# Optimization experiments

Measured on AMD Instinct MI355X. Metric: run time of the kernel, lower is better.

The kernel has to match this reference:

```python
import jax, jax.numpy as jnp
import numpy as np

EMBED_DIM = 256
SEQ_LEN = 4096
BATCH = 8
ALPHA = 0.99


def setup_inputs() -> dict:
    key = jax.random.key(0)
    k_x, k_w, k_b = jax.random.split(key, 3)
    x = jax.random.normal(k_x, (BATCH, SEQ_LEN, EMBED_DIM), dtype=jnp.float32)
    # nn.Linear(embed_dim, 3*embed_dim): store as [d, 3d] so y = x @ Wqkv + bqkv
    Wqkv = jax.random.normal(k_w, (EMBED_DIM, 3 * EMBED_DIM), dtype=jnp.float32) * (EMBED_DIM ** -0.5)
    bqkv = jax.random.normal(k_b, (3 * EMBED_DIM,), dtype=jnp.float32) * 0.02
    return {"x": x, "Wqkv": Wqkv, "bqkv": bqkv}


def reference(x, Wqkv, bqkv):
    bs, sl, d = x.shape
    qkv = x @ Wqkv + bqkv                      # [bs, sl, 3d]
    q, k, v = jnp.split(qkv, 3, axis=-1)       # each [bs, sl, d]
    # causal * exponential-decay mask: M[i, j] = alpha**(i-j) for j <= i else 0
    i = jnp.arange(sl, dtype=jnp.float32)
    M = jnp.where(i[:, None] >= i[None, :],
                  jnp.power(jnp.float32(ALPHA), i[:, None] - i[None, :]),
                  0.0)                          # [sl, sl]
    scores = jnp.einsum('bqd,bkd->bqk', q, k) / jnp.sqrt(jnp.float32(d))
    out = jnp.einsum('bqk,bkd->bqd', scores * M, v)
    return out
```

## Files before the change

kernel.cpp:

```cpp
#include <hip/hip_runtime.h>

typedef __bf16 bf16x8 __attribute__((ext_vector_type(8)));
typedef float f32x4 __attribute__((ext_vector_type(4)));
typedef unsigned short u16;
typedef unsigned int u32;
typedef u16 u16x4 __attribute__((ext_vector_type(4)));
typedef u16 u16x8 __attribute__((ext_vector_type(8)));

#define L2ALPHA (-0.014499569f)
#define WIN 1024

static __device__ __forceinline__ u16 f2bf(float f) {
    u32 u = __builtin_bit_cast(u32, f);
    return (u16)((u + 0x7FFFu + ((u >> 16) & 1u)) >> 16);
}

static __device__ __forceinline__ void gl2lds16(const void* g, void* l) {
    __builtin_amdgcn_global_load_lds(
        (const __attribute__((address_space(1))) u32*)g,
        (__attribute__((address_space(3))) u32*)l, 16, 0, 0);
}

__global__ __launch_bounds__(256, 2) void proj_kernel(
        const float* __restrict__ x, const float* __restrict__ Wq,
        const float* __restrict__ bias,
        u16* __restrict__ qb, u16* __restrict__ kb, u16* __restrict__ vb)
{
    __shared__ __align__(16) u16 Bs[32 * 128 * 8];
    __shared__ __align__(16) u16 As[4][32 * 40];

    const int tid = threadIdx.x, lane = tid & 63, w = tid >> 6;
    const int l = blockIdx.x;
    const int nb = l % 6;
    const int mt = l / 6;
    const int m0 = mt * 128, n0 = nb * 128;
    const int m = lane & 15, quad = lane >> 4;

    {
        const int col = tid & 127;
        const int khalf = tid >> 7;
        #pragma unroll
        for (int s = 0; s < 32; ++s) {
            int k0 = (khalf + 2 * s) * 4;
            u16x4 h;
            #pragma unroll
            for (int i = 0; i < 4; ++i)
                h[i] = f2bf(Wq[(k0 + i) * 768 + n0 + col]);
            *(u16x4*)&Bs[((k0 >> 3) * 128 + col) * 8 + (k0 & 7)] = h;
        }
    }
    __syncthreads();

    const int r = lane & 31, h = lane >> 5;
    const float* xrow = x + (size_t)(m0 + w * 32 + r) * 256 + h * 16;
    u16* As_w = &As[w][0];

    f32x4 acc[2][8];
    #pragma unroll
    for (int rt = 0; rt < 2; ++rt)
        #pragma unroll
        for (int ct = 0; ct < 8; ++ct)
            acc[rt][ct] = f32x4{0.f, 0.f, 0.f, 0.f};

    float4 g0 = *(const float4*)(xrow + 0);
    float4 g1 = *(const float4*)(xrow + 4);
    float4 g2 = *(const float4*)(xrow + 8);
    float4 g3 = *(const float4*)(xrow + 12);

    for (int kt = 0; kt < 8; ++kt) {
        u16x8 ha, hb;
        ha[0]=f2bf(g0.x); ha[1]=f2bf(g0.y); ha[2]=f2bf(g0.z); ha[3]=f2bf(g0.w);
        ha[4]=f2bf(g1.x); ha[5]=f2bf(g1.y); ha[6]=f2bf(g1.z); ha[7]=f2bf(g1.w);
        hb[0]=f2bf(g2.x); hb[1]=f2bf(g2.y); hb[2]=f2bf(g2.z); hb[3]=f2bf(g2.w);
        hb[4]=f2bf(g3.x); hb[5]=f2bf(g3.y); hb[6]=f2bf(g3.z); hb[7]=f2bf(g3.w);
        *(u16x8*)&As_w[r * 40 + h * 16]     = ha;
        *(u16x8*)&As_w[r * 40 + h * 16 + 8] = hb;

        if (kt < 7) {
            const float* xn = xrow + (kt + 1) * 32;
            g0 = *(const float4*)(xn + 0);
            g1 = *(const float4*)(xn + 4);
            g2 = *(const float4*)(xn + 8);
            g3 = *(const float4*)(xn + 12);
        }

        asm volatile("s_waitcnt lgkmcnt(0)" ::: "memory");

        bf16x8 af[2], bfr[8];
        #pragma unroll
        for (int rt = 0; rt < 2; ++rt)
            af[rt] = *(const bf16x8*)&As_w[(rt * 16 + m) * 40 + quad * 8];
        #pragma unroll
        for (int ct = 0; ct < 8; ++ct)
            bfr[ct] = *(const bf16x8*)&Bs[((kt * 4 + quad) * 128 + ct * 16 + m) * 8];
        #pragma unroll
        for (int rt = 0; rt < 2; ++rt)
            #pragma unroll
            for (int ct = 0; ct < 8; ++ct)
                acc[rt][ct] = __builtin_amdgcn_mfma_f32_16x16x32_bf16(
                    af[rt], bfr[ct], acc[rt][ct], 0, 0, 0);
    }

    const int b = m0 >> 12;
    const int jbase = (m0 & 4095) + w * 32;
    const int d0 = (nb & 1) * 128;

    if (nb < 2) {
        #pragma unroll
        for (int rt = 0; rt < 2; ++rt)
            #pragma unroll
            for (int ct = 0; ct < 8; ++ct) {
                int coll = ct * 16 + m;
                float bv = bias[d0 + coll];
                #pragma unroll
                for (int rr = 0; rr < 4; ++rr) {
                    int row = m0 + w * 32 + rt * 16 + quad * 4 + rr;
                    qb[(size_t)row * 256 + d0 + coll] = f2bf((acc[rt][ct][rr] + bv) * 0.0625f);
                }
            }
    } else if (nb < 4) {
        #pragma unroll
        for (int rt = 0; rt < 2; ++rt)
            #pragma unroll
            for (int ct = 0; ct < 8; ++ct) {
                int d = d0 + ct * 16 + m;
                float bv = bias[256 + d];
                int k8 = d >> 5, qk = (d >> 3) & 3, e = d & 7;
                #pragma unroll
                for (int rr = 0; rr < 4; ++rr) {
                    int j = jbase + rt * 16 + quad * 4 + rr;
                    int jt = j >> 5, jj = j & 31;
                    kb[((((size_t)(b * 128 + jt) * 2 + (jj & 1)) * 8 + k8) * 64 + qk * 16 + (jj >> 1)) * 8 + e]
                        = f2bf(acc[rt][ct][rr] + bv);
                }
            }
    } else {
        #pragma unroll
        for (int rt = 0; rt < 2; ++rt)
            #pragma unroll
            for (int ct = 0; ct < 8; ++ct) {
                int d = d0 + ct * 16 + m;
                float bv = bias[512 + d];
                int dt = d >> 4, mv = d & 15;
                int j = jbase + rt * 16 + quad * 4;
                int jt = j >> 5, qv = (j >> 3) & 3, e0 = j & 7;
                u16x4 hv;
                #pragma unroll
                for (int rr = 0; rr < 4; ++rr) hv[rr] = f2bf(acc[rt][ct][rr] + bv);
                *(u16x4*)&vb[(((size_t)(b * 128 + jt) * 16 + dt) * 64 + qv * 16 + mv) * 8 + e0] = hv;
            }
    }
}

__global__ __launch_bounds__(512, 2) void attn_kernel(
        const u16* __restrict__ qb, const u16* __restrict__ kb,
        const u16* __restrict__ vb, float* __restrict__ out)
{
    __shared__ __align__(16) u16 KV[2][2][16384];
    __shared__ __align__(16) u16 Ps[8 * 32 * 40];

    const int tid = threadIdx.x, lane = tid & 63, w = tid >> 6;
    const int wp = w & 3, par = w >> 2;
    const int l = blockIdx.x;
    const int b = l & 7;
    const int m0 = (l >> 3) * 128;
    const int qrow0 = m0 + wp * 32;
    const int m = lane & 15, quad = lane >> 4;
    const size_t rowbase = (size_t)b * 4096;
    const size_t pbase = (size_t)b * 128;

    bf16x8 qf[2][8];
    #pragma unroll
    for (int rg = 0; rg < 2; ++rg)
        #pragma unroll
        for (int k8 = 0; k8 < 8; ++k8)
            qf[rg][k8] = *(const bf16x8*)(qb + (rowbase + qrow0 + rg * 16 + m) * 256 + k8 * 32 + quad * 8);

    float Arow[2][4];
    #pragma unroll
    for (int rg = 0; rg < 2; ++rg)
        #pragma unroll
        for (int rr = 0; rr < 4; ++rr)
            Arow[rg][rr] = __builtin_amdgcn_exp2f((float)(rg * 16 + quad * 4 + rr) * L2ALPHA);
    const float Em0 = __builtin_amdgcn_exp2f((float)(-2 * m) * L2ALPHA);
    const float Em1 = __builtin_amdgcn_exp2f((float)(-2 * m - 1) * L2ALPHA);

    f32x4 acc[2][16];
    #pragma unroll
    for (int rg = 0; rg < 2; ++rg)
        #pragma unroll
        for (int dt = 0; dt < 16; ++dt)
            acc[rg][dt] = f32x4{0.f, 0.f, 0.f, 0.f};

    int t0 = (m0 - WIN) >> 5; if (t0 < 0) t0 = 0;
    const int t1 = (m0 >> 5) + 3;
    const int nIter = (t1 - t0 + 2) >> 1;

    {
        const u16* kpA = kb + (pbase + t0) * 8192;
        const u16* vpA = vb + (pbase + t0) * 8192;
        const u16* kpB = kpA + 8192;
        const u16* vpB = vpA + 8192;
        #pragma unroll
        for (int s = 0; s < 2; ++s) {
            int c = tid + 512 * s;
            gl2lds16(kpA + (size_t)c * 8, &KV[0][0][c * 8]);
            gl2lds16(vpA + (size_t)c * 8, &KV[0][0][8192 + c * 8]);
            gl2lds16(kpB + (size_t)c * 8, &KV[0][1][c * 8]);
            gl2lds16(vpB + (size_t)c * 8, &KV[0][1][8192 + c * 8]);
        }
    }

    int p = 0;
    for (int it = 0; it < nIter; ++it) {
        __syncthreads();
        if (it + 1 < nIter) {
            const int ta = t0 + 2 * (it + 1);
            const bool haveB = (ta + 1 <= t1);
            const u16* kpA = kb + (pbase + ta) * 8192;
            const u16* vpA = vb + (pbase + ta) * 8192;
            #pragma unroll
            for (int s = 0; s < 2; ++s) {
                int c = tid + 512 * s;
                gl2lds16(kpA + (size_t)c * 8, &KV[p ^ 1][0][c * 8]);
                gl2lds16(vpA + (size_t)c * 8, &KV[p ^ 1][0][8192 + c * 8]);
                if (haveB) {
                    gl2lds16(kpA + 8192 + (size_t)c * 8, &KV[p ^ 1][1][c * 8]);
                    gl2lds16(vpA + 8192 + (size_t)c * 8, &KV[p ^ 1][1][8192 + c * 8]);
                }
            }
        }

        const int t = t0 + 2 * it + par;
        const int j0 = t * 32;
        if (t <= t1 && j0 <= qrow0 + 31 && j0 + (WIN + 31) >= qrow0) {
            const u16* Kt = &KV[p][par][0];
            const u16* Vt = &KV[p][par][8192];

            const float base = __builtin_amdgcn_exp2f((float)(qrow0 - j0) * L2ALPHA);
            const float C0 = base * Em0, C1 = base * Em1;
            const bool diag = (j0 == qrow0);

            f32x4 sA0{0.f,0.f,0.f,0.f}, sA1{0.f,0.f,0.f,0.f};
            f32x4 sB0{0.f,0.f,0.f,0.f}, sB1{0.f,0.f,0.f,0.f};
            #pragma unroll
            for (int k8 = 0; k8 < 8; ++k8) {
                bf16x8 bf0 = *(const bf16x8*)&Kt[(k8 * 64 + lane) * 8];
                sA0 = __builtin_amdgcn_mfma_f32_16x16x32_bf16(qf[0][k8], bf0, sA0, 0, 0, 0);
                sA1 = __builtin_amdgcn_mfma_f32_16x16x32_bf16(qf[1][k8], bf0, sA1, 0, 0, 0);
            }
            #pragma unroll
            for (int k8 = 0; k8 < 8; ++k8) {
                bf16x8 bf1 = *(const bf16x8*)&Kt[((8 + k8) * 64 + lane) * 8];
                sB0 = __builtin_amdgcn_mfma_f32_16x16x32_bf16(qf[0][k8], bf1, sB0, 0, 0, 0);
                sB1 = __builtin_amdgcn_mfma_f32_16x16x32_bf16(qf[1][k8], bf1, sB1, 0, 0, 0);
            }

            if (diag) {
                #pragma unroll
                for (int rg = 0; rg < 2; ++rg) {
                    f32x4 sh0 = rg ? sA1 : sA0;
                    f32x4 sh1 = rg ? sB1 : sB0;
                    #pragma unroll
                    for (int rr = 0; rr < 4; ++rr) {
                        int ioff = rg * 16 + quad * 4 + rr;
                        int dd0 = ioff - 2 * m;
                        float w0 = (dd0 >= 0) ? Arow[rg][rr] * C0 : 0.0f;
                        float w1 = (dd0 >= 1) ? Arow[rg][rr] * C1 : 0.0f;
                        int rowb = (w * 32 + ioff) * 40;
                        u32 pv = (u32)f2bf(sh0[rr] * w0) | ((u32)f2bf(sh1[rr] * w1) << 16);
                        *(u32*)&Ps[rowb + 2 * m] = pv;
                    }
                }
            } else {
                #pragma unroll
                for (int rg = 0; rg < 2; ++rg) {
                    f32x4 sh0 = rg ? sA1 : sA0;
                    f32x4 sh1 = rg ? sB1 : sB0;
                    #pragma unroll
                    for (int rr = 0; rr < 4; ++rr) {
                        int ioff = rg * 16 + quad * 4 + rr;
                        float w0 = Arow[rg][rr] * C0;
                        float w1 = Arow[rg][rr] * C1;
                        int rowb = (w * 32 + ioff) * 40;
                        u32 pv = (u32)f2bf(sh0[rr] * w0) | ((u32)f2bf(sh1[rr] * w1) << 16);
                        *(u32*)&Ps[rowb + 2 * m] = pv;
                    }
                }
            }
            asm volatile("s_waitcnt lgkmcnt(0)" ::: "memory");

            bf16x8 pa0 = *(const bf16x8*)&Ps[(w * 32 + m) * 40 + quad * 8];
            bf16x8 pa1 = *(const bf16x8*)&Ps[(w * 32 + 16 + m) * 40 + quad * 8];

            #pragma unroll
            for (int dt = 0; dt < 16; ++dt) {
                bf16x8 vf = *(const bf16x8*)&Vt[(dt * 64 + lane) * 8];
                acc[0][dt] = __builtin_amdgcn_mfma_f32_16x16x32_bf16(pa0, vf, acc[0][dt], 0, 0, 0);
                acc[1][dt] = __builtin_amdgcn_mfma_f32_16x16x32_bf16(pa1, vf, acc[1][dt], 0, 0, 0);
            }
        }
        p ^= 1;
    }

    __syncthreads();
    float* Comb = (float*)&KV[0][0][0];
    if (par == 1) {
        float* dst = Comb + (size_t)wp * 8192 + lane * 128;
        #pragma unroll
        for (int rg = 0; rg < 2; ++rg)
            #pragma unroll
            for (int dt = 0; dt < 16; ++dt) {
                int idx = rg * 16 + dt;
                *(f32x4*)(dst + (idx ^ (lane & 7)) * 4) = acc[rg][dt];
            }
    }
    __syncthreads();
    if (par == 0) {
        const float* src = Comb + (size_t)wp * 8192 + lane * 128;
        #pragma unroll
        for (int rg = 0; rg < 2; ++rg)
            #pragma unroll
            for (int dt = 0; dt < 16; ++dt) {
                int idx = rg * 16 + dt;
                f32x4 o = acc[rg][dt] + *(const f32x4*)(src + (idx ^ (lane & 7)) * 4);
                #pragma unroll
                for (int rr = 0; rr < 4; ++rr)
                    out[(rowbase + qrow0 + rg * 16 + quad * 4 + rr) * 256 + dt * 16 + m] = o[rr];
            }
    }
}

extern "C" void kernel_launch(void* const* d_in, const int* in_sizes, int n_in,
                              void* d_out, int out_size, void* d_ws, size_t ws_size,
                              hipStream_t stream) {
    (void)in_sizes; (void)n_in; (void)out_size; (void)ws_size;
    const float* x    = (const float*)d_in[0];
    const float* Wq   = (const float*)d_in[1];
    const float* bias = (const float*)d_in[2];
    float* outp = (float*)d_out;

    const size_t per = (size_t)8 * 4096 * 256;
    u16* qb = (u16*)d_ws;
    u16* kb = qb + per;
    u16* vb = kb + per;

    proj_kernel<<<1536, 256, 0, stream>>>(x, Wq, bias, qb, kb, vb);
    attn_kernel<<<256, 512, 0, stream>>>(qb, kb, vb, outp);
}
```

Measured before the change: 208.9 us.

## Load V directly to registers and triple-buffer K in LDS

V tiles are no longer staged through LDS. Each wave loads its V fragments straight from global memory into registers, while K keeps an LDS ring of three buffers loaded two iterations ahead. Barriers are replaced with explicit vmcnt waits plus s_barrier, and the final cross-wave reduction runs in two halves so it fits the smaller LDS footprint. The aim is to halve LDS traffic and capacity use and to deepen prefetch, at the cost of more VGPR pressure and fragile hand-counted vmcnt values.

```diff
diff --git a/kernel.cpp b/kernel.cpp
--- a/kernel.cpp
+++ b/kernel.cpp
@@ -156,7 +156,7 @@
         const u16* __restrict__ qb, const u16* __restrict__ kb,
         const u16* __restrict__ vb, float* __restrict__ out)
 {
-    __shared__ __align__(16) u16 KV[2][2][16384];
+    __shared__ __align__(16) u16 KR[3][2][8192];
     __shared__ __align__(16) u16 Ps[8 * 32 * 40];
 
     const int tid = threadIdx.x, lane = tid & 63, w = tid >> 6;
@@ -196,46 +196,49 @@
     const int t1 = (m0 >> 5) + 3;
     const int nIter = (t1 - t0 + 2) >> 1;
 
-    {
-        const u16* kpA = kb + (pbase + t0) * 8192;
-        const u16* vpA = vb + (pbase + t0) * 8192;
-        const u16* kpB = kpA + 8192;
-        const u16* vpB = vpA + 8192;
-        #pragma unroll
-        for (int s = 0; s < 2; ++s) {
-            int c = tid + 512 * s;
-            gl2lds16(kpA + (size_t)c * 8, &KV[0][0][c * 8]);
-            gl2lds16(vpA + (size_t)c * 8, &KV[0][0][8192 + c * 8]);
-            gl2lds16(kpB + (size_t)c * 8, &KV[0][1][c * 8]);
-            gl2lds16(vpB + (size_t)c * 8, &KV[0][1][8192 + c * 8]);
-        }
-    }
-
-    int p = 0;
+    #define STAGE_K(itx)                                                    \
+        do {                                                                \
+            const int ta_ = t0 + 2 * (itx);                                 \
+            const int buf_ = (itx) % 3;                                     \
+            const u16* kpA_ = kb + (pbase + ta_) * 8192;                    \
+            const u16* kpB_ = kpA_ + 8192;                                  \
+            _Pragma("unroll")                                               \
+            for (int s_ = 0; s_ < 2; ++s_) {                                \
+                int c_ = tid + 512 * s_;                                    \
+                gl2lds16(kpA_ + (size_t)c_ * 8, &KR[buf_][0][c_ * 8]);      \
+                gl2lds16(kpB_ + (size_t)c_ * 8, &KR[buf_][1][c_ * 8]);      \
+            }                                                               \
+        } while (0)
+
+    STAGE_K(0);
+    STAGE_K(1);
+
     for (int it = 0; it < nIter; ++it) {
-        __syncthreads();
-        if (it + 1 < nIter) {
-            const int ta = t0 + 2 * (it + 1);
-            const bool haveB = (ta + 1 <= t1);
-            const u16* kpA = kb + (pbase + ta) * 8192;
-            const u16* vpA = vb + (pbase + ta) * 8192;
-            #pragma unroll
-            for (int s = 0; s < 2; ++s) {
-                int c = tid + 512 * s;
-                gl2lds16(kpA + (size_t)c * 8, &KV[p ^ 1][0][c * 8]);
-                gl2lds16(vpA + (size_t)c * 8, &KV[p ^ 1][0][8192 + c * 8]);
-                if (haveB) {
-                    gl2lds16(kpA + 8192 + (size_t)c * 8, &KV[p ^ 1][1][c * 8]);
-                    gl2lds16(vpA + 8192 + (size_t)c * 8, &KV[p ^ 1][1][8192 + c * 8]);
-                }
-            }
-        }
-
         const int t = t0 + 2 * it + par;
         const int j0 = t * 32;
-        if (t <= t1 && j0 <= qrow0 + 31 && j0 + (WIN + 31) >= qrow0) {
-            const u16* Kt = &KV[p][par][0];
-            const u16* Vt = &KV[p][par][8192];
+        const bool valid = (t <= t1) && (j0 <= qrow0 + 31) && (j0 + (WIN + 31) >= qrow0);
+
+        bf16x8 vf[16];
+        if (valid) {
+            const u16* Vg = vb + (pbase + (size_t)t) * 8192 + lane * 8;
+            #pragma unroll
+            for (int dt = 0; dt < 16; ++dt)
+                vf[dt] = *(const bf16x8*)(Vg + dt * 512);
+        }
+
+        if (valid) {
+            if (it + 1 < nIter) asm volatile("s_waitcnt vmcnt(20)" ::: "memory");
+            else                asm volatile("s_waitcnt vmcnt(16)" ::: "memory");
+        } else {
+            if (it + 1 < nIter) asm volatile("s_waitcnt vmcnt(4)" ::: "memory");
+            else                asm volatile("s_waitcnt vmcnt(0)" ::: "memory");
+        }
+        __builtin_amdgcn_s_barrier();
+
+        if (it + 2 < nIter) STAGE_K(it + 2);
+
+        if (valid) {
+            const u16* Kt = &KR[it % 3][par][0];
 
             const float base = __builtin_amdgcn_exp2f((float)(qrow0 - j0) * L2ALPHA);
             const float C0 = base * Em0, C1 = base * Em1;
@@ -295,39 +298,39 @@
 
             #pragma unroll
             for (int dt = 0; dt < 16; ++dt) {
-                bf16x8 vf = *(const bf16x8*)&Vt[(dt * 64 + lane) * 8];
-                acc[0][dt] = __builtin_amdgcn_mfma_f32_16x16x32_bf16(pa0, vf, acc[0][dt], 0, 0, 0);
-                acc[1][dt] = __builtin_amdgcn_mfma_f32_16x16x32_bf16(pa1, vf, acc[1][dt], 0, 0, 0);
-            }
-        }
-        p ^= 1;
-    }
-
-    __syncthreads();
-    float* Comb = (float*)&KV[0][0][0];
-    if (par == 1) {
-        float* dst = Comb + (size_t)wp * 8192 + lane * 128;
-        #pragma unroll
-        for (int rg = 0; rg < 2; ++rg)
+                acc[0][dt] = __builtin_amdgcn_mfma_f32_16x16x32_bf16(pa0, vf[dt], acc[0][dt], 0, 0, 0);
+                acc[1][dt] = __builtin_amdgcn_mfma_f32_16x16x32_bf16(pa1, vf[dt], acc[1][dt], 0, 0, 0);
+            }
+        }
+    }
+
+    asm volatile("s_waitcnt lgkmcnt(0)" ::: "memory");
+    __builtin_amdgcn_s_barrier();
+    float* Comb = (float*)&KR[0][0][0];
+    #pragma unroll
+    for (int rg = 0; rg < 2; ++rg) {
+        if (par == 1) {
+            float* dst = Comb + (size_t)wp * 4096 + lane * 64;
+            #pragma unroll
+            for (int dt = 0; dt < 16; ++dt)
+                *(f32x4*)(dst + (dt ^ (lane & 7)) * 4) = acc[rg][dt];
+        }
+        asm volatile("s_waitcnt lgkmcnt(0)" ::: "memory");
+        __builtin_amdgcn_s_barrier();
+        if (par == 0) {
+            const float* src = Comb + (size_t)wp * 4096 + lane * 64;
             #pragma unroll
             for (int dt = 0; dt < 16; ++dt) {
-                int idx = rg * 16 + dt;
-                *(f32x4*)(dst + (idx ^ (lane & 7)) * 4) = acc[rg][dt];
-            }
-    }
-    __syncthreads();
-    if (par == 0) {
-        const float* src = Comb + (size_t)wp * 8192 + lane * 128;
-        #pragma unroll
-        for (int rg = 0; rg < 2; ++rg)
-            #pragma unroll
-            for (int dt = 0; dt < 16; ++dt) {
-                int idx = rg * 16 + dt;
-                f32x4 o = acc[rg][dt] + *(const f32x4*)(src + (idx ^ (lane & 7)) * 4);
+                f32x4 o = acc[rg][dt] + *(const f32x4*)(src + (dt ^ (lane & 7)) * 4);
                 #pragma unroll
                 for (int rr = 0; rr < 4; ++rr)
                     out[(rowbase + qrow0 + rg * 16 + quad * 4 + rr) * 256 + dt * 16 + m] = o[rr];
             }
+        }
+        if (rg == 0) {
+            asm volatile("s_waitcnt lgkmcnt(0)" ::: "memory");
+            __builtin_amdgcn_s_barrier();
+        }
     }
 }
 
```

Result: slower. 381.3 us (+82.5%).

## Prefetch two KV tile-pairs ahead with explicit vmcnt waits and raw barriers

Applied to the files above, without the earlier changes.

Restructures the K/V staging loop so two tile-pairs are in flight at once. The next-next pair is issued after each compute step, and each iteration waits with a partial s_waitcnt vmcnt(8) instead of a full __syncthreads drain. This is meant to let global-to-LDS loads overlap more compute and to avoid the full memory-counter drain that __syncthreads implies. The nIter formula changes and the haveB and t<=t1 guards are dropped, so every stage always loads both tiles of a pair. The manual waitcnt values depend on the exact number of loads issued per stage, which is fragile.

```diff
diff --git a/kernel.cpp b/kernel.cpp
--- a/kernel.cpp
+++ b/kernel.cpp
@@ -175,6 +175,7 @@
         #pragma unroll
         for (int k8 = 0; k8 < 8; ++k8)
             qf[rg][k8] = *(const bf16x8*)(qb + (rowbase + qrow0 + rg * 16 + m) * 256 + k8 * 32 + quad * 8);
+    asm volatile("s_waitcnt vmcnt(0)" ::: "memory");
 
     float Arow[2][4];
     #pragma unroll
@@ -194,46 +195,35 @@
 
     int t0 = (m0 - WIN) >> 5; if (t0 < 0) t0 = 0;
     const int t1 = (m0 >> 5) + 3;
-    const int nIter = (t1 - t0 + 2) >> 1;
-
-    {
-        const u16* kpA = kb + (pbase + t0) * 8192;
-        const u16* vpA = vb + (pbase + t0) * 8192;
-        const u16* kpB = kpA + 8192;
-        const u16* vpB = vpA + 8192;
-        #pragma unroll
-        for (int s = 0; s < 2; ++s) {
-            int c = tid + 512 * s;
-            gl2lds16(kpA + (size_t)c * 8, &KV[0][0][c * 8]);
-            gl2lds16(vpA + (size_t)c * 8, &KV[0][0][8192 + c * 8]);
-            gl2lds16(kpB + (size_t)c * 8, &KV[0][1][c * 8]);
-            gl2lds16(vpB + (size_t)c * 8, &KV[0][1][8192 + c * 8]);
-        }
-    }
-
-    int p = 0;
+    const int nIter = (t1 - t0 + 1) >> 1;
+
+    #define STAGE_PAIR(ix, bf)                                              \
+        do {                                                                \
+            const u16* kpA_ = kb + (pbase + t0 + 2 * (ix)) * 8192;          \
+            const u16* vpA_ = vb + (pbase + t0 + 2 * (ix)) * 8192;          \
+            _Pragma("unroll")                                               \
+            for (int s_ = 0; s_ < 2; ++s_) {                                \
+                int c_ = tid + 512 * s_;                       \
+                gl2lds16(kpA_ + (size_t)c_ * 8, &KV[bf][0][c_ * 8]);        \
+                gl2lds16(vpA_ + (size_t)c_ * 8, &KV[bf][0][8192 + c_ * 8]); \
+                gl2lds16(kpA_ + 8192 + (size_t)c_ * 8, &KV[bf][1][c_ * 8]); \
+                gl2lds16(vpA_ + 8192 + (size_t)c_ * 8, &KV[bf][1][8192 + c_ * 8]); \
+            }                                                               \
+        } while (0)
+
+    STAGE_PAIR(0, 0);
+    STAGE_PAIR(1, 1);
+
     for (int it = 0; it < nIter; ++it) {
-        __syncthreads();
-        if (it + 1 < nIter) {
-            const int ta = t0 + 2 * (it + 1);
-            const bool haveB = (ta + 1 <= t1);
-            const u16* kpA = kb + (pbase + ta) * 8192;
-            const u16* vpA = vb + (pbase + ta) * 8192;
-            #pragma unroll
-            for (int s = 0; s < 2; ++s) {
-                int c = tid + 512 * s;
-                gl2lds16(kpA + (size_t)c * 8, &KV[p ^ 1][0][c * 8]);
-                gl2lds16(vpA + (size_t)c * 8, &KV[p ^ 1][0][8192 + c * 8]);
-                if (haveB) {
-                    gl2lds16(kpA + 8192 + (size_t)c * 8, &KV[p ^ 1][1][c * 8]);
-                    gl2lds16(vpA + 8192 + (size_t)c * 8, &KV[p ^ 1][1][8192 + c * 8]);
-                }
-            }
-        }
+        const int p = it & 1;
+        if (it + 1 < nIter) asm volatile("s_waitcnt vmcnt(8)" ::: "memory");
+        else                asm volatile("s_waitcnt vmcnt(0)" ::: "memory");
+        __builtin_amdgcn_s_barrier();
+        asm volatile("" ::: "memory");
 
         const int t = t0 + 2 * it + par;
         const int j0 = t * 32;
-        if (t <= t1 && j0 <= qrow0 + 31 && j0 + (WIN + 31) >= qrow0) {
+        if (j0 <= qrow0 + 31 && j0 + (WIN + 31) >= qrow0) {
             const u16* Kt = &KV[p][par][0];
             const u16* Vt = &KV[p][par][8192];
 
@@ -267,9 +257,8 @@
                         int dd0 = ioff - 2 * m;
                         float w0 = (dd0 >= 0) ? Arow[rg][rr] * C0 : 0.0f;
                         float w1 = (dd0 >= 1) ? Arow[rg][rr] * C1 : 0.0f;
-                        int rowb = (w * 32 + ioff) * 40;
                         u32 pv = (u32)f2bf(sh0[rr] * w0) | ((u32)f2bf(sh1[rr] * w1) << 16);
-                        *(u32*)&Ps[rowb + 2 * m] = pv;
+                        *(u32*)&Ps[(w * 32 + ioff) * 40 + 2 * m] = pv;
                     }
                 }
             } else {
@@ -282,9 +271,8 @@
                         int ioff = rg * 16 + quad * 4 + rr;
                         float w0 = Arow[rg][rr] * C0;
                         float w1 = Arow[rg][rr] * C1;
-                        int rowb = (w * 32 + ioff) * 40;
                         u32 pv = (u32)f2bf(sh0[rr] * w0) | ((u32)f2bf(sh1[rr] * w1) << 16);
-                        *(u32*)&Ps[rowb + 2 * m] = pv;
+                        *(u32*)&Ps[(w * 32 + ioff) * 40 + 2 * m] = pv;
                     }
                 }
             }
@@ -300,10 +288,14 @@
                 acc[1][dt] = __builtin_amdgcn_mfma_f32_16x16x32_bf16(pa1, vf, acc[1][dt], 0, 0, 0);
             }
         }
-        p ^= 1;
-    }
-
-    __syncthreads();
+
+        asm volatile("" ::: "memory");
+        __builtin_amdgcn_s_barrier();
+        if (it + 2 < nIter) STAGE_PAIR(it + 2, p);
+    }
+
+    asm volatile("" ::: "memory");
+    __builtin_amdgcn_s_barrier();
     float* Comb = (float*)&KV[0][0][0];
     if (par == 1) {
         float* dst = Comb + (size_t)wp * 8192 + lane * 128;
@@ -315,7 +307,8 @@
                 *(f32x4*)(dst + (idx ^ (lane & 7)) * 4) = acc[rg][dt];
             }
     }
-    __syncthreads();
+    asm volatile("s_waitcnt lgkmcnt(0)" ::: "memory");
+    __builtin_amdgcn_s_barrier();
     if (par == 0) {
         const float* src = Comb + (size_t)wp * 8192 + lane * 128;
         #pragma unroll
```

Measured after the change: 218.5 us. 4.6% more time.
